# Kernel tuning notes

Measured on AMD Instinct MI355X. Metric: run time of the kernel, lower is better.

The kernel has to match this reference:

```python
import jax, jax.numpy as jnp
import numpy as np

B, T, D, HS = 4, 2048, 1024, 64


def setup_inputs() -> dict:
    key = jax.random.key(0)
    ks = jax.random.split(key, 8)
    s = 0.02
    return {
        "x": jax.random.normal(ks[0], (B, T, D), dtype=jnp.float32),
        "wq": jax.random.normal(ks[1], (D, HS), dtype=jnp.float32) * s,
        "bq": jax.random.normal(ks[2], (HS,), dtype=jnp.float32) * s,
        "wk": jax.random.normal(ks[3], (D, HS), dtype=jnp.float32) * s,
        "bk": jax.random.normal(ks[4], (HS,), dtype=jnp.float32) * s,
        "wv": jax.random.normal(ks[5], (D, HS), dtype=jnp.float32) * s,
        "bv": jax.random.normal(ks[6], (HS,), dtype=jnp.float32) * s,
        "rel_pos_embd": jax.random.normal(ks[7], (T, T, HS), dtype=jnp.float32) * s,
    }


def reference(x, wq, bq, wk, bk, wv, bv, rel_pos_embd):
    # x: [B,T,D]
    q = jnp.einsum("btd,dh->bth", x, wq) + bq  # [B,T,HS]
    k = jnp.einsum("btd,dh->bth", x, wk) + bk
    v = jnp.einsum("btd,dh->bth", x, wv) + bv
    hs = k.shape[-1]
    # faithful to torch: scores = QK^T / hs**(-0.5) == QK^T * sqrt(hs)
    scores = jnp.einsum("bth,bvh->btv", q, k) * jnp.sqrt(jnp.float32(hs))
    # relative-position bias (mask=False branch)
    rel = jnp.einsum("btc,tvc->btv", q, rel_pos_embd[:q.shape[1], :q.shape[1]])
    att = jax.nn.softmax(scores + rel, axis=-1)  # [B,T,T]
    return jnp.einsum("btv,bvh->bth", att, v)  # [B,T,HS]
```

## Files before the change

### kernel.cpp

```cpp
#include <hip/hip_runtime.h>

#define B_ 4
#define T_ 2048
#define D_ 1024
#define HS_ 64

typedef __attribute__((ext_vector_type(4))) float f32x4;
typedef __attribute__((ext_vector_type(8))) short bf16x8;
typedef __attribute__((ext_vector_type(4))) unsigned short u16x4;
typedef __attribute__((ext_vector_type(4))) unsigned int u32x4;

__device__ __forceinline__ unsigned short f2bf(float f) {
  unsigned int u = __float_as_uint(f);
  u += 0x7FFFu + ((u >> 16) & 1u);
  return (unsigned short)(u >> 16);
}
__device__ __forceinline__ float bf2f(unsigned short s) {
  return __uint_as_float(((unsigned int)s) << 16);
}

__global__ void kconv_kernel(const float* __restrict__ wq, const float* __restrict__ wk,
                             const float* __restrict__ wv,
                             unsigned short* __restrict__ wTh, unsigned short* __restrict__ wTl) {
  int gid = blockIdx.x * 256 + threadIdx.x;
  int n = gid >> 10, d = gid & 1023;
  float v;
  if (n < 64)        v = wq[d * 64 + n];
  else if (n < 128)  v = 8.0f * wk[d * 64 + (n - 64)];
  else               v = wv[d * 64 + (n - 128)];
  unsigned short h = f2bf(v);
  wTh[gid] = h;
  wTl[gid] = f2bf(v - __uint_as_float(((unsigned int)h) << 16));
}

__global__ __launch_bounds__(256) void kproj_kernel(
    const float* __restrict__ x, const unsigned short* __restrict__ wTh,
    const unsigned short* __restrict__ wTl,
    const float* __restrict__ bq, const float* __restrict__ bk, const float* __restrict__ bv,
    float* __restrict__ qw, float* __restrict__ k8w, unsigned short* __restrict__ vbw) {
  __shared__ unsigned short xh[32 * 32], xl[32 * 32];
  __shared__ unsigned short wh[192 * 32], wl[192 * 32];
  const int tid = threadIdx.x;
  const int m0 = blockIdx.x * 32;
  const int lane = tid & 63, wid = tid >> 6;
  const int mf = wid & 1, np = wid >> 1;
  const int r15 = lane & 15, u = lane >> 4;

  f32x4 xv;
  f32x4 wvh[3], wvl[3];
  auto issue = [&](int k0) {
    xv = *(const f32x4*)&x[(m0 + (tid >> 3)) * 1024 + k0 + (tid & 7) * 4];
#pragma unroll
    for (int i = 0; i < 3; ++i) {
      int c8 = i * 256 + tid;
      wvh[i] = *(const f32x4*)&wTh[(c8 >> 2) * 1024 + k0 + (c8 & 3) * 8];
      wvl[i] = *(const f32x4*)&wTl[(c8 >> 2) * 1024 + k0 + (c8 & 3) * 8];
    }
  };
  auto commit = [&]() {
    u16x4 hhv, llv;
#pragma unroll
    for (int c = 0; c < 4; ++c) {
      unsigned short h = f2bf(xv[c]);
      hhv[c] = h;
      llv[c] = f2bf(xv[c] - __uint_as_float(((unsigned int)h) << 16));
    }
    *(u16x4*)&xh[(tid >> 3) * 32 + (tid & 7) * 4] = hhv;
    *(u16x4*)&xl[(tid >> 3) * 32 + (tid & 7) * 4] = llv;
#pragma unroll
    for (int i = 0; i < 3; ++i) {
      int c8 = i * 256 + tid;
      *(f32x4*)&wh[c8 * 8] = wvh[i];
      *(f32x4*)&wl[c8 * 8] = wvl[i];
    }
  };

  f32x4 z = {0.f, 0.f, 0.f, 0.f};
  f32x4 acc[6] = {z, z, z, z, z, z};
  issue(0);
  for (int kt = 0; kt < 32; ++kt) {
    __syncthreads();
    commit();
    __syncthreads();
    if (kt + 1 < 32) issue((kt + 1) * 32);
    bf16x8 ah = *(const bf16x8*)&xh[(mf * 16 + r15) * 32 + u * 8];
    bf16x8 al = *(const bf16x8*)&xl[(mf * 16 + r15) * 32 + u * 8];
#pragma unroll
    for (int nf = 0; nf < 6; ++nf) {
      int nr = np * 96 + nf * 16 + r15;
      bf16x8 bh = *(const bf16x8*)&wh[nr * 32 + u * 8];
      bf16x8 bl = *(const bf16x8*)&wl[nr * 32 + u * 8];
      acc[nf] = __builtin_amdgcn_mfma_f32_16x16x32_bf16(ah, bh, acc[nf], 0, 0, 0);
      acc[nf] = __builtin_amdgcn_mfma_f32_16x16x32_bf16(ah, bl, acc[nf], 0, 0, 0);
      acc[nf] = __builtin_amdgcn_mfma_f32_16x16x32_bf16(al, bh, acc[nf], 0, 0, 0);
    }
  }
#pragma unroll
  for (int nf = 0; nf < 6; ++nf) {
    const int n = np * 96 + nf * 16 + r15;
#pragma unroll
    for (int r = 0; r < 4; ++r) {
      const int m = m0 + mf * 16 + u * 4 + r;
      float val = acc[nf][r];
      if (n < 64) {
        qw[m * 64 + n] = val + bq[n];
      } else if (n < 128) {
        k8w[m * 64 + (n - 64)] = val + 8.0f * bk[n - 64];
      } else {
        int h = n - 128;
        vbw[m * 64 + h] = f2bf(val + bv[h]);
      }
    }
  }
}

__global__ __launch_bounds__(256, 2) void kfused(
    const float* __restrict__ qw, const float* __restrict__ k8w,
    const unsigned short* __restrict__ vbw, const float* __restrict__ rel,
    float* __restrict__ Oh, float* __restrict__ ml2) {
  __shared__ float kl[2][32 * 68];
  __shared__ unsigned short vt_[2][32 * 76];
  const int tid = threadIdx.x;
  const int tt = blockIdx.x >> 1, vh = blockIdx.x & 1;
  const int t0 = tt * 8;
  const int vbase = vh * 1024;
  const int wid = tid >> 6;
  const int tl = (tid >> 5) & 1;
  const int vl = (tid >> 2) & 7;
  const int hq = tid & 3;
  const int tloc = wid * 2 + tl;
  const int tg = t0 + tloc;

  f32x4 qr[4][4];
#pragma unroll
  for (int b = 0; b < 4; ++b)
#pragma unroll
    for (int j = 0; j < 4; ++j)
      qr[b][j] = *(const f32x4*)&qw[((b << 11) + tg) * 64 + hq * 16 + j * 4];

  const float* relrow = rel + (size_t)tg * 131072 + hq * 16;

  f32x4 rA[4], rB[4];
  f32x4 stk[2];
  f32x4 stv;

#define ISSUE_REL(DST, VT) do {                                           \
    const float* p_ = relrow + (size_t)((VT) + vl) * 64;                  \
    DST[0] = *(const f32x4*)(p_);                                         \
    DST[1] = *(const f32x4*)(p_ + 4);                                     \
    DST[2] = *(const f32x4*)(p_ + 8);                                     \
    DST[3] = *(const f32x4*)(p_ + 12);                                    \
  } while (0)

  auto issue_kv = [&](int vt) {
#pragma unroll
    for (int i = 0; i < 2; ++i) {
      int c4 = i * 256 + tid;
      int pr = c4 >> 4, c = c4 & 15;
      stk[i] = *(const f32x4*)&k8w[(pr >> 3) * 131072 + (vt + (pr & 7)) * 64 + c * 4];
    }
    {
      int pr = tid >> 3, cc = tid & 7;
      stv = *(const f32x4*)&vbw[(((pr >> 3) << 11) + vt + (pr & 7)) * 64 + cc * 8];
    }
  };
  auto commit_kv = [&](int buf) {
#pragma unroll
    for (int i = 0; i < 2; ++i) {
      int c4 = i * 256 + tid;
      int pr = c4 >> 4, c = c4 & 15;
      *(f32x4*)&kl[buf][pr * 68 + c * 4] = stk[i];
    }
    {
      int pr = tid >> 3, cc = tid & 7;
      const u16x4* pv = (const u16x4*)&stv;
      *(u16x4*)&vt_[buf][pr * 76 + cc * 8] = pv[0];
      *(u16x4*)&vt_[buf][pr * 76 + cc * 8 + 4] = pv[1];
    }
  };

  float o[64];
#pragma unroll
  for (int h = 0; h < 64; ++h) o[h] = 0.0f;
  float mrun = -3.0e38f, lrun = 0.0f;

#define PHASE_BARRIER() do {                                              \
    asm volatile("s_waitcnt lgkmcnt(0)" ::: "memory");                    \
    __builtin_amdgcn_s_barrier();                                         \
    asm volatile("" ::: "memory");                                        \
  } while (0)

#define COMPUTE(RC, BUF) do {                                             \
    f32x4 z4 = {0.f, 0.f, 0.f, 0.f};                                      \
    f32x4 a0 = z4, a1 = z4, a2 = z4, a3 = z4;                             \
    const float* krow = &kl[BUF][vl * 68];                                \
    _Pragma("unroll")                                                     \
    for (int j = 0; j < 4; ++j) {                                         \
      int c = (hq * 4 + j) * 4;                                           \
      f32x4 r4 = RC[j];                                                   \
      f32x4 kb0 = *(const f32x4*)&krow[c];                                \
      f32x4 kb1 = *(const f32x4*)&krow[544 + c];                          \
      f32x4 kb2 = *(const f32x4*)&krow[1088 + c];                         \
      f32x4 kb3 = *(const f32x4*)&krow[1632 + c];                         \
      a0 += qr[0][j] * (kb0 + r4);                                        \
      a1 += qr[1][j] * (kb1 + r4);                                        \
      a2 += qr[2][j] * (kb2 + r4);                                        \
      a3 += qr[3][j] * (kb3 + r4);                                        \
    }                                                                     \
    float s0 = a0[0] + a0[1] + a0[2] + a0[3];                             \
    float s1 = a1[0] + a1[1] + a1[2] + a1[3];                             \
    float s2 = a2[0] + a2[1] + a2[2] + a2[3];                             \
    float s3 = a3[0] + a3[1] + a3[2] + a3[3];                             \
    s0 += __shfl_xor(s0, 1); s0 += __shfl_xor(s0, 2);                     \
    s1 += __shfl_xor(s1, 1); s1 += __shfl_xor(s1, 2);                     \
    s2 += __shfl_xor(s2, 1); s2 += __shfl_xor(s2, 2);                     \
    s3 += __shfl_xor(s3, 1); s3 += __shfl_xor(s3, 2);                     \
    float s = (hq == 0) ? s0 : (hq == 1) ? s1 : (hq == 2) ? s2 : s3;      \
    float mx = s;                                                         \
    mx = fmaxf(mx, __shfl_xor(mx, 4));                                    \
    mx = fmaxf(mx, __shfl_xor(mx, 8));                                    \
    mx = fmaxf(mx, __shfl_xor(mx, 16));                                   \
    if (__any(mx > mrun + 5.0f)) {        \
      float mnew = fmaxf(mrun, mx);                                       \
      float alpha = __expf(mrun - mnew);                                  \
      lrun *= alpha;                                                      \
      _Pragma("unroll")                                                   \
      for (int h = 0; h < 64; ++h) o[h] *= alpha;                         \
      mrun = mnew;                                                        \
    }                                                                     \
    float p = __expf(s - mrun);                                           \
    float ps_ = p;                                                        \
    ps_ += __shfl_xor(ps_, 4);                                            \
    ps_ += __shfl_xor(ps_, 8);                                            \
    ps_ += __shfl_xor(ps_, 16);                                           \
    lrun += ps_;                                                          \
    const unsigned short* vrow = &vt_[BUF][(hq * 8 + vl) * 76];           \
    _Pragma("unroll")                                                     \
    for (int k = 0; k < 16; ++k) {                                        \
      u16x4 vv = *(const u16x4*)&vrow[k * 4];                             \
      o[k * 4 + 0] = fmaf(p, bf2f(vv[0]), o[k * 4 + 0]);                  \
      o[k * 4 + 1] = fmaf(p, bf2f(vv[1]), o[k * 4 + 1]);                  \
      o[k * 4 + 2] = fmaf(p, bf2f(vv[2]), o[k * 4 + 2]);                  \
      o[k * 4 + 3] = fmaf(p, bf2f(vv[3]), o[k * 4 + 3]);                  \
    }                                                                     \
  } while (0)

  ISSUE_REL(rA, vbase);
  issue_kv(vbase);
  commit_kv(0);
  PHASE_BARRIER();

  int cur = 0;
  for (int it2 = 0; it2 < 64; ++it2) {
    const int vt = vbase + it2 * 16;
    {
      ISSUE_REL(rB, vt + 8);
      issue_kv(vt + 8);
      COMPUTE(rA, cur);
      commit_kv(cur ^ 1);
      PHASE_BARRIER();
      cur ^= 1;
    }
    {
      const bool more = (it2 + 1 < 64);
      if (more) {
        ISSUE_REL(rA, vt + 16);
        issue_kv(vt + 16);
      }
      COMPUTE(rB, cur);
      if (more) commit_kv(cur ^ 1);
      PHASE_BARRIER();
      cur ^= 1;
    }
  }

  float n32[32];
#pragma unroll
  for (int j = 0; j < 32; ++j) {
    float send = (vl & 4) ? o[j] : o[j + 32];
    float t = __shfl_xor(send, 16);
    float keep = (vl & 4) ? o[j + 32] : o[j];
    n32[j] = keep + t;
  }
  float n16[16];
#pragma unroll
  for (int j = 0; j < 16; ++j) {
    float send = (vl & 2) ? n32[j] : n32[j + 16];
    float t = __shfl_xor(send, 8);
    float keep = (vl & 2) ? n32[j + 16] : n32[j];
    n16[j] = keep + t;
  }
  float n8[8];
#pragma unroll
  for (int j = 0; j < 8; ++j) {
    float send = (vl & 1) ? n16[j] : n16[j + 8];
    float t = __shfl_xor(send, 4);
    float keep = (vl & 1) ? n16[j + 8] : n16[j];
    n8[j] = keep + t;
  }

  const int orow = (vh * 4 + hq) * 2048 + tg;
  f32x4 w0 = {n8[0], n8[1], n8[2], n8[3]};
  f32x4 w1 = {n8[4], n8[5], n8[6], n8[7]};
  *(f32x4*)&Oh[orow * 64 + vl * 8] = w0;
  *(f32x4*)&Oh[orow * 64 + vl * 8 + 4] = w1;
  if (vl == 0) {
    ml2[orow * 2] = mrun;
    ml2[orow * 2 + 1] = lrun;
  }
#undef ISSUE_REL
#undef COMPUTE
#undef PHASE_BARRIER
}

__global__ __launch_bounds__(256) void kcomb(
    const float* __restrict__ Oh, const float* __restrict__ ml2,
    float* __restrict__ O) {
  int gid = blockIdx.x * 256 + threadIdx.x;
  int row = gid >> 4, hc = gid & 15;
  float m0 = ml2[row * 2], l0 = ml2[row * 2 + 1];
  float m1 = ml2[(8192 + row) * 2], l1 = ml2[(8192 + row) * 2 + 1];
  float m = fmaxf(m0, m1);
  float c0 = __expf(m0 - m), c1 = __expf(m1 - m);
  float linv = 1.0f / (c0 * l0 + c1 * l1);
  f32x4 o0 = *(const f32x4*)&Oh[row * 64 + hc * 4];
  f32x4 o1 = *(const f32x4*)&Oh[(8192 + row) * 64 + hc * 4];
  f32x4 r;
#pragma unroll
  for (int j = 0; j < 4; ++j) r[j] = (c0 * o0[j] + c1 * o1[j]) * linv;
  *(f32x4*)&O[row * 64 + hc * 4] = r;
}

extern "C" void kernel_launch(void* const* d_in, const int* in_sizes, int n_in,
                              void* d_out, int out_size, void* d_ws, size_t ws_size,
                              hipStream_t stream) {
  const float* x   = (const float*)d_in[0];
  const float* wq  = (const float*)d_in[1];
  const float* bq  = (const float*)d_in[2];
  const float* wk  = (const float*)d_in[3];
  const float* bk  = (const float*)d_in[4];
  const float* wv  = (const float*)d_in[5];
  const float* bv  = (const float*)d_in[6];
  const float* rel = (const float*)d_in[7];
  float* O = (float*)d_out;

  char* ws = (char*)d_ws;
  float* qw            = (float*)(ws);
  float* k8w           = (float*)(ws + 2097152);
  unsigned short* vbw  = (unsigned short*)(ws + 4194304);
  unsigned short* wTh  = (unsigned short*)(ws + 5242880);
  unsigned short* wTl  = (unsigned short*)(ws + 5636096);
  float* Oh            = (float*)(ws + 6291456);
  float* ml2           = (float*)(ws + 10485760);

  kconv_kernel<<<dim3(768), dim3(256), 0, stream>>>(wq, wk, wv, wTh, wTl);
  kproj_kernel<<<dim3(256), dim3(256), 0, stream>>>(x, wTh, wTl, bq, bk, bv, qw, k8w, vbw);
  kfused<<<dim3(512), dim3(256), 0, stream>>>(qw, k8w, vbw, rel, Oh, ml2);
  kcomb<<<dim3(512), dim3(256), 0, stream>>>(Oh, ml2, O);
}
```

Measured before the change: 381.3 us.

## Precompute QK^T scores with split-bf16 MFMA kernel and process 16 keys per step

```diff
diff --git a/kernel.cpp b/kernel.cpp
--- a/kernel.cpp
+++ b/kernel.cpp
@@ -37,7 +37,10 @@
     const float* __restrict__ x, const unsigned short* __restrict__ wTh,
     const unsigned short* __restrict__ wTl,
     const float* __restrict__ bq, const float* __restrict__ bk, const float* __restrict__ bv,
-    float* __restrict__ qw, float* __restrict__ k8w, unsigned short* __restrict__ vbw) {
+    float* __restrict__ qw,
+    unsigned short* __restrict__ qhb, unsigned short* __restrict__ qlb,
+    unsigned short* __restrict__ khb, unsigned short* __restrict__ klb,
+    unsigned short* __restrict__ vbw) {
   __shared__ unsigned short xh[32 * 32], xl[32 * 32];
   __shared__ unsigned short wh[192 * 32], wl[192 * 32];
   const int tid = threadIdx.x;
@@ -103,9 +106,16 @@
       const int m = m0 + mf * 16 + u * 4 + r;
       float val = acc[nf][r];
       if (n < 64) {
-        qw[m * 64 + n] = val + bq[n];
+        float qv = val + bq[n];
+        qw[m * 64 + n] = qv;
+        unsigned short h = f2bf(qv);
+        qhb[m * 64 + n] = h;
+        qlb[m * 64 + n] = f2bf(qv - __uint_as_float(((unsigned int)h) << 16));
       } else if (n < 128) {
-        k8w[m * 64 + (n - 64)] = val + 8.0f * bk[n - 64];
+        float kv = val + 8.0f * bk[n - 64];
+        unsigned short h = f2bf(kv);
+        khb[m * 64 + (n - 64)] = h;
+        klb[m * 64 + (n - 64)] = f2bf(kv - __uint_as_float(((unsigned int)h) << 16));
       } else {
         int h = n - 128;
         vbw[m * 64 + h] = f2bf(val + bv[h]);
@@ -114,12 +124,67 @@
   }
 }
 
+__global__ __launch_bounds__(256, 2) void kqk_kernel(
+    const unsigned short* __restrict__ qhb, const unsigned short* __restrict__ qlb,
+    const unsigned short* __restrict__ khb, const unsigned short* __restrict__ klb,
+    float* __restrict__ S0L) {
+  const int tid = threadIdx.x;
+  const int wid = tid >> 6, lane = tid & 63;
+  const int r15 = lane & 15, u = lane >> 4;
+  const int t0 = (blockIdx.x >> 3) * 16;
+  const int v0 = (blockIdx.x & 7) * 256 + wid * 64;
+
+  bf16x8 ah[4][2], al[4][2];
+#pragma unroll
+  for (int b = 0; b < 4; ++b)
+#pragma unroll
+    for (int ks = 0; ks < 2; ++ks) {
+      int off = ((b << 11) + t0 + r15) * 64 + ks * 32 + u * 8;
+      ah[b][ks] = *(const bf16x8*)&qhb[off];
+      al[b][ks] = *(const bf16x8*)&qlb[off];
+    }
+
+  f32x4 z = {0.f, 0.f, 0.f, 0.f};
+  f32x4 acc[4][4] = {{z,z,z,z},{z,z,z,z},{z,z,z,z},{z,z,z,z}};
+
+#pragma unroll
+  for (int s = 0; s < 4; ++s) {
+    const int v1 = v0 + s * 16;
+    bf16x8 bh[4][2], bl[4][2];
+#pragma unroll
+    for (int b = 0; b < 4; ++b)
+#pragma unroll
+      for (int ks = 0; ks < 2; ++ks) {
+        int off = ((b << 11) + v1 + r15) * 64 + ks * 32 + u * 8;
+        bh[b][ks] = *(const bf16x8*)&khb[off];
+        bl[b][ks] = *(const bf16x8*)&klb[off];
+      }
+#pragma unroll
+    for (int b = 0; b < 4; ++b)
+#pragma unroll
+      for (int ks = 0; ks < 2; ++ks) {
+        acc[s][b] = __builtin_amdgcn_mfma_f32_16x16x32_bf16(ah[b][ks], bh[b][ks], acc[s][b], 0, 0, 0);
+        acc[s][b] = __builtin_amdgcn_mfma_f32_16x16x32_bf16(ah[b][ks], bl[b][ks], acc[s][b], 0, 0, 0);
+        acc[s][b] = __builtin_amdgcn_mfma_f32_16x16x32_bf16(al[b][ks], bh[b][ks], acc[s][b], 0, 0, 0);
+      }
+  }
+#pragma unroll
+  for (int s = 0; s < 4; ++s) {
+#pragma unroll
+    for (int r = 0; r < 4; ++r) {
+      f32x4 pk = {acc[s][0][r], acc[s][1][r], acc[s][2][r], acc[s][3][r]};
+      size_t t = (size_t)(t0 + u * 4 + r);
+      size_t v = (size_t)(v0 + s * 16 + r15);
+      *(f32x4*)&S0L[(t * 2048 + v) * 4] = pk;
+    }
+  }
+}
+
 __global__ __launch_bounds__(256, 2) void kfused(
-    const float* __restrict__ qw, const float* __restrict__ k8w,
+    const float* __restrict__ qw, const float* __restrict__ S0L,
     const unsigned short* __restrict__ vbw, const float* __restrict__ rel,
     float* __restrict__ Oh, float* __restrict__ ml2) {
-  __shared__ float kl[2][32 * 68];
-  __shared__ unsigned short vt_[2][32 * 76];
+  __shared__ unsigned short vt_[2][64 * 74];
   const int tid = threadIdx.x;
   const int tt = blockIdx.x >> 1, vh = blockIdx.x & 1;
   const int t0 = tt * 8;
@@ -139,43 +204,39 @@
       qr[b][j] = *(const f32x4*)&qw[((b << 11) + tg) * 64 + hq * 16 + j * 4];
 
   const float* relrow = rel + (size_t)tg * 131072 + hq * 16;
-
-  f32x4 rA[4], rB[4];
-  f32x4 stk[2];
-  f32x4 stv;
-
-#define ISSUE_REL(DST, VT) do {                                           \
-    const float* p_ = relrow + (size_t)((VT) + vl) * 64;                  \
-    DST[0] = *(const f32x4*)(p_);                                         \
-    DST[1] = *(const f32x4*)(p_ + 4);                                     \
-    DST[2] = *(const f32x4*)(p_ + 8);                                     \
-    DST[3] = *(const f32x4*)(p_ + 12);                                    \
+  const float* s0row = S0L + (size_t)tg * 8192 + hq;
+
+  f32x4 rA[8], rB[8];
+  float s0A[2], s0B[2];
+  f32x4 stv[2];
+
+#define ISSUE_REL(DST, S0D, VT) do {                                      \
+    const float* p0_ = relrow + (size_t)((VT) + vl) * 64;                 \
+    const float* p1_ = relrow + (size_t)((VT) + vl + 8) * 64;             \
+    DST[0] = *(const f32x4*)(p0_);      DST[1] = *(const f32x4*)(p0_ + 4);\
+    DST[2] = *(const f32x4*)(p0_ + 8);  DST[3] = *(const f32x4*)(p0_ +12);\
+    DST[4] = *(const f32x4*)(p1_);      DST[5] = *(const f32x4*)(p1_ + 4);\
+    DST[6] = *(const f32x4*)(p1_ + 8);  DST[7] = *(const f32x4*)(p1_ +12);\
+    S0D[0] = s0row[((VT) + vl) * 4];                                      \
+    S0D[1] = s0row[((VT) + vl + 8) * 4];                                  \
   } while (0)
 
-  auto issue_kv = [&](int vt) {
+  auto issue_v = [&](int vt) {
 #pragma unroll
     for (int i = 0; i < 2; ++i) {
-      int c4 = i * 256 + tid;
-      int pr = c4 >> 4, c = c4 & 15;
-      stk[i] = *(const f32x4*)&k8w[(pr >> 3) * 131072 + (vt + (pr & 7)) * 64 + c * 4];
-    }
-    {
-      int pr = tid >> 3, cc = tid & 7;
-      stv = *(const f32x4*)&vbw[(((pr >> 3) << 11) + vt + (pr & 7)) * 64 + cc * 8];
+      int c8 = i * 256 + tid;
+      int pr = c8 >> 3, cc = c8 & 7;
+      stv[i] = *(const f32x4*)&vbw[(((pr >> 4) << 11) + vt + (pr & 15)) * 64 + cc * 8];
     }
   };
-  auto commit_kv = [&](int buf) {
+  auto commit_v = [&](int buf) {
 #pragma unroll
     for (int i = 0; i < 2; ++i) {
-      int c4 = i * 256 + tid;
-      int pr = c4 >> 4, c = c4 & 15;
-      *(f32x4*)&kl[buf][pr * 68 + c * 4] = stk[i];
-    }
-    {
-      int pr = tid >> 3, cc = tid & 7;
-      const u16x4* pv = (const u16x4*)&stv;
-      *(u16x4*)&vt_[buf][pr * 76 + cc * 8] = pv[0];
-      *(u16x4*)&vt_[buf][pr * 76 + cc * 8 + 4] = pv[1];
+      int c8 = i * 256 + tid;
+      int pr = c8 >> 3, cc = c8 & 7;
+      const u16x4* pv = (const u16x4*)&stv[i];
+      *(u16x4*)&vt_[buf][pr * 74 + cc * 8] = pv[0];
+      *(u16x4*)&vt_[buf][pr * 74 + cc * 8 + 4] = pv[1];
     }
   };
 
@@ -190,33 +251,40 @@
     asm volatile("" ::: "memory");                                        \
   } while (0)
 
-#define COMPUTE(RC, BUF) do {                                             \
+#define COMPUTE(RC, S0R, BUF) do {                                        \
     f32x4 z4 = {0.f, 0.f, 0.f, 0.f};                                      \
     f32x4 a0 = z4, a1 = z4, a2 = z4, a3 = z4;                             \
-    const float* krow = &kl[BUF][vl * 68];                                \
+    f32x4 c0 = z4, c1 = z4, c2 = z4, c3 = z4;                             \
     _Pragma("unroll")                                                     \
     for (int j = 0; j < 4; ++j) {                                         \
-      int c = (hq * 4 + j) * 4;                                           \
-      f32x4 r4 = RC[j];                                                   \
-      f32x4 kb0 = *(const f32x4*)&krow[c];                                \
-      f32x4 kb1 = *(const f32x4*)&krow[544 + c];                          \
-      f32x4 kb2 = *(const f32x4*)&krow[1088 + c];                         \
-      f32x4 kb3 = *(const f32x4*)&krow[1632 + c];                         \
-      a0 += qr[0][j] * (kb0 + r4);                                        \
-      a1 += qr[1][j] * (kb1 + r4);                                        \
-      a2 += qr[2][j] * (kb2 + r4);                                        \
-      a3 += qr[3][j] * (kb3 + r4);                                        \
+      a0 += qr[0][j] * RC[j];                                             \
+      a1 += qr[1][j] * RC[j];                                             \
+      a2 += qr[2][j] * RC[j];                                             \
+      a3 += qr[3][j] * RC[j];                                             \
+      c0 += qr[0][j] * RC[4 + j];                                         \
+      c1 += qr[1][j] * RC[4 + j];                                         \
+      c2 += qr[2][j] * RC[4 + j];                                         \
+      c3 += qr[3][j] * RC[4 + j];                                         \
     }                                                                     \
-    float s0 = a0[0] + a0[1] + a0[2] + a0[3];                             \
-    float s1 = a1[0] + a1[1] + a1[2] + a1[3];                             \
-    float s2 = a2[0] + a2[1] + a2[2] + a2[3];                             \
-    float s3 = a3[0] + a3[1] + a3[2] + a3[3];                             \
-    s0 += __shfl_xor(s0, 1); s0 += __shfl_xor(s0, 2);                     \
-    s1 += __shfl_xor(s1, 1); s1 += __shfl_xor(s1, 2);                     \
-    s2 += __shfl_xor(s2, 1); s2 += __shfl_xor(s2, 2);                     \
-    s3 += __shfl_xor(s3, 1); s3 += __shfl_xor(s3, 2);                     \
-    float s = (hq == 0) ? s0 : (hq == 1) ? s1 : (hq == 2) ? s2 : s3;      \
-    float mx = s;                                                         \
+    float sa0 = a0[0] + a0[1] + a0[2] + a0[3];                            \
+    float sa1 = a1[0] + a1[1] + a1[2] + a1[3];                            \
+    float sa2 = a2[0] + a2[1] + a2[2] + a2[3];                            \
+    float sa3 = a3[0] + a3[1] + a3[2] + a3[3];                            \
+    float sb0 = c0[0] + c0[1] + c0[2] + c0[3];                            \
+    float sb1 = c1[0] + c1[1] + c1[2] + c1[3];                            \
+    float sb2 = c2[0] + c2[1] + c2[2] + c2[3];                            \
+    float sb3 = c3[0] + c3[1] + c3[2] + c3[3];                            \
+    sa0 += __shfl_xor(sa0, 1); sa0 += __shfl_xor(sa0, 2);                 \
+    sa1 += __shfl_xor(sa1, 1); sa1 += __shfl_xor(sa1, 2);                 \
+    sa2 += __shfl_xor(sa2, 1); sa2 += __shfl_xor(sa2, 2);                 \
+    sa3 += __shfl_xor(sa3, 1); sa3 += __shfl_xor(sa3, 2);                 \
+    sb0 += __shfl_xor(sb0, 1); sb0 += __shfl_xor(sb0, 2);                 \
+    sb1 += __shfl_xor(sb1, 1); sb1 += __shfl_xor(sb1, 2);                 \
+    sb2 += __shfl_xor(sb2, 1); sb2 += __shfl_xor(sb2, 2);                 \
+    sb3 += __shfl_xor(sb3, 1); sb3 += __shfl_xor(sb3, 2);                 \
+    float sA = ((hq == 0) ? sa0 : (hq == 1) ? sa1 : (hq == 2) ? sa2 : sa3) + S0R[0]; \
+    float sB = ((hq == 0) ? sb0 : (hq == 1) ? sb1 : (hq == 2) ? sb2 : sb3) + S0R[1]; \
+    float mx = fmaxf(sA, sB);                                             \
     mx = fmaxf(mx, __shfl_xor(mx, 4));                                    \
     mx = fmaxf(mx, __shfl_xor(mx, 8));                                    \
     mx = fmaxf(mx, __shfl_xor(mx, 16));                                   \
@@ -228,47 +296,54 @@
       for (int h = 0; h < 64; ++h) o[h] *= alpha;                         \
       mrun = mnew;                                                        \
     }                                                                     \
-    float p = __expf(s - mrun);                                           \
-    float ps_ = p;                                                        \
+    float p0 = __expf(sA - mrun);                                         \
+    float p1 = __expf(sB - mrun);                                         \
+    float ps_ = p0 + p1;                                                  \
     ps_ += __shfl_xor(ps_, 4);                                            \
     ps_ += __shfl_xor(ps_, 8);                                            \
     ps_ += __shfl_xor(ps_, 16);                                           \
     lrun += ps_;                                                          \
-    const unsigned short* vrow = &vt_[BUF][(hq * 8 + vl) * 76];           \
+    const unsigned short* vrA = &vt_[BUF][(hq * 16 + vl) * 74];           \
+    const unsigned short* vrB = &vt_[BUF][(hq * 16 + vl + 8) * 74];       \
     _Pragma("unroll")                                                     \
     for (int k = 0; k < 16; ++k) {                                        \
-      u16x4 vv = *(const u16x4*)&vrow[k * 4];                             \
-      o[k * 4 + 0] = fmaf(p, bf2f(vv[0]), o[k * 4 + 0]);                  \
-      o[k * 4 + 1] = fmaf(p, bf2f(vv[1]), o[k * 4 + 1]);                  \
-      o[k * 4 + 2] = fmaf(p, bf2f(vv[2]), o[k * 4 + 2]);                  \
-      o[k * 4 + 3] = fmaf(p, bf2f(vv[3]), o[k * 4 + 3]);                  \
+      u16x4 va = *(const u16x4*)&vrA[k * 4];                              \
+      u16x4 vb = *(const u16x4*)&vrB[k * 4];                              \
+      o[k * 4 + 0] = fmaf(p0, bf2f(va[0]), o[k * 4 + 0]);                 \
+      o[k * 4 + 1] = fmaf(p0, bf2f(va[1]), o[k * 4 + 1]);                 \
+      o[k * 4 + 2] = fmaf(p0, bf2f(va[2]), o[k * 4 + 2]);                 \
+      o[k * 4 + 3] = fmaf(p0, bf2f(va[3]), o[k * 4 + 3]);                 \
+      o[k * 4 + 0] = fmaf(p1, bf2f(vb[0]), o[k * 4 + 0]);                 \
+      o[k * 4 + 1] = fmaf(p1, bf2f(vb[1]), o[k * 4 + 1]);                 \
+      o[k * 4 + 2] = fmaf(p1, bf2f(vb[2]), o[k * 4 + 2]);                 \
+      o[k * 4 + 3] = fmaf(p1, bf2f(vb[3]), o[k * 4 + 3]);                 \
     }                                                                     \
   } while (0)
 
-  ISSUE_REL(rA, vbase);
-  issue_kv(vbase);
-  commit_kv(0);
+  ISSUE_REL(rA, s0A, vbase);
+  issue_v(vbase);
+  commit_v(0);
   PHASE_BARRIER();
 
   int cur = 0;
-  for (int it2 = 0; it2 < 64; ++it2) {
-    const int vt = vbase + it2 * 16;
+  for (int it2 = 0; it2 < 32; ++it2) {
+    const int vt = vbase + it2 * 32;
     {
-      ISSUE_REL(rB, vt + 8);
-      issue_kv(vt + 8);
-      COMPUTE(rA, cur);
-      commit_kv(cur ^ 1);
+      ISSUE_REL(rB, s0B, vt + 16);
+      issue_v(vt + 16);
+      COMPUTE(rA, s0A, cur);
+      commit_v(cur ^ 1);
       PHASE_BARRIER();
       cur ^= 1;
     }
     {
-      const bool more = (it2 + 1 < 64);
+      const bool more = (it2 + 1 < 32);
       if (more) {
-        ISSUE_REL(rA, vt + 16);
-        issue_kv(vt + 16);
+        ISSUE_REL(rA, s0A, vt + 32);
+        issue_v(vt + 32);
       }
-      COMPUTE(rB, cur);
-      if (more) commit_kv(cur ^ 1);
+      COMPUTE(rB, s0B, cur);
+      if (more) commit_v(cur ^ 1);
       PHASE_BARRIER();
       cur ^= 1;
     }
@@ -345,16 +420,22 @@
   float* O = (float*)d_out;
 
   char* ws = (char*)d_ws;
-  float* qw            = (float*)(ws);
-  float* k8w           = (float*)(ws + 2097152);
-  unsigned short* vbw  = (unsigned short*)(ws + 4194304);
-  unsigned short* wTh  = (unsigned short*)(ws + 5242880);
-  unsigned short* wTl  = (unsigned short*)(ws + 5636096);
-  float* Oh            = (float*)(ws + 6291456);
-  float* ml2           = (float*)(ws + 10485760);
+  float* S0L           = (float*)(ws);
+  unsigned short* wTh  = (unsigned short*)(ws);
+  unsigned short* wTl  = (unsigned short*)(ws + 393216);
+  float* qw            = (float*)(ws + 67108864);
+  unsigned short* vbw  = (unsigned short*)(ws + 69206016);
+  unsigned short* qhb  = (unsigned short*)(ws + 70254592);
+  unsigned short* qlb  = (unsigned short*)(ws + 71303168);
+  unsigned short* khb  = (unsigned short*)(ws + 72351744);
+  unsigned short* klb  = (unsigned short*)(ws + 73400320);
+  float* Oh            = (float*)(ws + 74448896);
+  float* ml2           = (float*)(ws + 78643200);
 
   kconv_kernel<<<dim3(768), dim3(256), 0, stream>>>(wq, wk, wv, wTh, wTl);
-  kproj_kernel<<<dim3(256), dim3(256), 0, stream>>>(x, wTh, wTl, bq, bk, bv, qw, k8w, vbw);
-  kfused<<<dim3(512), dim3(256), 0, stream>>>(qw, k8w, vbw, rel, Oh, ml2);
+  kproj_kernel<<<dim3(256), dim3(256), 0, stream>>>(x, wTh, wTl, bq, bk, bv,
+                                                    qw, qhb, qlb, khb, klb, vbw);
+  kqk_kernel<<<dim3(1024), dim3(256), 0, stream>>>(qhb, qlb, khb, klb, S0L);
+  kfused<<<dim3(512), dim3(256), 0, stream>>>(qw, S0L, vbw, rel, Oh, ml2);
   kcomb<<<dim3(512), dim3(256), 0, stream>>>(Oh, ml2, O);
 }
```

Measured after the change: 1.044 ms. 2.74x slower.

## Split attention key range into four partitions and combine four partial results

Applied to the files above, without the earlier changes.

```diff
diff --git a/kernel.cpp b/kernel.cpp
--- a/kernel.cpp
+++ b/kernel.cpp
@@ -119,11 +119,11 @@
     const unsigned short* __restrict__ vbw, const float* __restrict__ rel,
     float* __restrict__ Oh, float* __restrict__ ml2) {
   __shared__ float kl[2][32 * 68];
-  __shared__ unsigned short vt_[2][32 * 76];
+  __shared__ unsigned short vt_[2][32 * 74];
   const int tid = threadIdx.x;
-  const int tt = blockIdx.x >> 1, vh = blockIdx.x & 1;
+  const int tt = blockIdx.x >> 2, vq = blockIdx.x & 3;
   const int t0 = tt * 8;
-  const int vbase = vh * 1024;
+  const int vbase = vq * 512;
   const int wid = tid >> 6;
   const int tl = (tid >> 5) & 1;
   const int vl = (tid >> 2) & 7;
@@ -174,8 +174,8 @@
     {
       int pr = tid >> 3, cc = tid & 7;
       const u16x4* pv = (const u16x4*)&stv;
-      *(u16x4*)&vt_[buf][pr * 76 + cc * 8] = pv[0];
-      *(u16x4*)&vt_[buf][pr * 76 + cc * 8 + 4] = pv[1];
+      *(u16x4*)&vt_[buf][pr * 74 + cc * 8] = pv[0];
+      *(u16x4*)&vt_[buf][pr * 74 + cc * 8 + 4] = pv[1];
     }
   };
 
@@ -234,7 +234,7 @@
     ps_ += __shfl_xor(ps_, 8);                                            \
     ps_ += __shfl_xor(ps_, 16);                                           \
     lrun += ps_;                                                          \
-    const unsigned short* vrow = &vt_[BUF][(hq * 8 + vl) * 76];           \
+    const unsigned short* vrow = &vt_[BUF][(hq * 8 + vl) * 74];           \
     _Pragma("unroll")                                                     \
     for (int k = 0; k < 16; ++k) {                                        \
       u16x4 vv = *(const u16x4*)&vrow[k * 4];                             \
@@ -251,7 +251,7 @@
   PHASE_BARRIER();
 
   int cur = 0;
-  for (int it2 = 0; it2 < 64; ++it2) {
+  for (int it2 = 0; it2 < 32; ++it2) {
     const int vt = vbase + it2 * 16;
     {
       ISSUE_REL(rB, vt + 8);
@@ -262,7 +262,7 @@
       cur ^= 1;
     }
     {
-      const bool more = (it2 + 1 < 64);
+      const bool more = (it2 + 1 < 32);
       if (more) {
         ISSUE_REL(rA, vt + 16);
         issue_kv(vt + 16);
@@ -299,14 +299,15 @@
     n8[j] = keep + t;
   }
 
-  const int orow = (vh * 4 + hq) * 2048 + tg;
+  const int orow = hq * 2048 + tg;
+  float* Ohq = Oh + (size_t)vq * 524288;
   f32x4 w0 = {n8[0], n8[1], n8[2], n8[3]};
   f32x4 w1 = {n8[4], n8[5], n8[6], n8[7]};
-  *(f32x4*)&Oh[orow * 64 + vl * 8] = w0;
-  *(f32x4*)&Oh[orow * 64 + vl * 8 + 4] = w1;
+  *(f32x4*)&Ohq[orow * 64 + vl * 8] = w0;
+  *(f32x4*)&Ohq[orow * 64 + vl * 8 + 4] = w1;
   if (vl == 0) {
-    ml2[orow * 2] = mrun;
-    ml2[orow * 2 + 1] = lrun;
+    ml2[(vq * 8192 + orow) * 2] = mrun;
+    ml2[(vq * 8192 + orow) * 2 + 1] = lrun;
   }
 #undef ISSUE_REL
 #undef COMPUTE
@@ -318,16 +319,28 @@
     float* __restrict__ O) {
   int gid = blockIdx.x * 256 + threadIdx.x;
   int row = gid >> 4, hc = gid & 15;
-  float m0 = ml2[row * 2], l0 = ml2[row * 2 + 1];
-  float m1 = ml2[(8192 + row) * 2], l1 = ml2[(8192 + row) * 2 + 1];
-  float m = fmaxf(m0, m1);
-  float c0 = __expf(m0 - m), c1 = __expf(m1 - m);
-  float linv = 1.0f / (c0 * l0 + c1 * l1);
-  f32x4 o0 = *(const f32x4*)&Oh[row * 64 + hc * 4];
-  f32x4 o1 = *(const f32x4*)&Oh[(8192 + row) * 64 + hc * 4];
+  float mq[4], lq[4];
+  float m = -3.0e38f;
+#pragma unroll
+  for (int q = 0; q < 4; ++q) {
+    mq[q] = ml2[(q * 8192 + row) * 2];
+    lq[q] = ml2[(q * 8192 + row) * 2 + 1];
+    m = fmaxf(m, mq[q]);
+  }
+  float den = 0.0f;
+  f32x4 acc = {0.f, 0.f, 0.f, 0.f};
+#pragma unroll
+  for (int q = 0; q < 4; ++q) {
+    float c = __expf(mq[q] - m);
+    den = fmaf(c, lq[q], den);
+    f32x4 oq = *(const f32x4*)&Oh[(size_t)q * 524288 + row * 64 + hc * 4];
+#pragma unroll
+    for (int j = 0; j < 4; ++j) acc[j] = fmaf(c, oq[j], acc[j]);
+  }
+  float inv = 1.0f / den;
   f32x4 r;
 #pragma unroll
-  for (int j = 0; j < 4; ++j) r[j] = (c0 * o0[j] + c1 * o1[j]) * linv;
+  for (int j = 0; j < 4; ++j) r[j] = acc[j] * inv;
   *(f32x4*)&O[row * 64 + hc * 4] = r;
 }
 
@@ -351,10 +364,10 @@
   unsigned short* wTh  = (unsigned short*)(ws + 5242880);
   unsigned short* wTl  = (unsigned short*)(ws + 5636096);
   float* Oh            = (float*)(ws + 6291456);
-  float* ml2           = (float*)(ws + 10485760);
+  float* ml2           = (float*)(ws + 14680064);
 
   kconv_kernel<<<dim3(768), dim3(256), 0, stream>>>(wq, wk, wv, wTh, wTl);
   kproj_kernel<<<dim3(256), dim3(256), 0, stream>>>(x, wTh, wTl, bq, bk, bv, qw, k8w, vbw);
-  kfused<<<dim3(512), dim3(256), 0, stream>>>(qw, k8w, vbw, rel, Oh, ml2);
+  kfused<<<dim3(1024), dim3(256), 0, stream>>>(qw, k8w, vbw, rel, Oh, ml2);
   kcomb<<<dim3(512), dim3(256), 0, stream>>>(Oh, ml2, O);
 }
```

Result: slower. 712.7 us (+86.9%).
